# Performance work log

Measured on AMD Instinct MI355X. Metric: run time of the kernel, lower is better.

Reference implementation:

```python
import jax, jax.numpy as jnp
import numpy as np

N_USERS = 50000
N_ENTITIES = 150000
N_NODES = N_USERS + N_ENTITIES
N_EDGES = 3200000
BATCH = 4096
EPS = 1e-12  # F.normalize eps


def setup_inputs() -> dict:
    key = jax.random.key(0)
    ks = jax.random.split(key, 16)
    s = 0.1  # xavier-ish scale for small dims
    return {
        "user_w": jax.random.normal(ks[0], (N_USERS, 64), jnp.float32) * s,
        "entity_w": jax.random.normal(ks[1], (N_ENTITIES, 64), jnp.float32) * s,
        "W1a": jax.random.normal(ks[2], (64, 64), jnp.float32) * s,
        "b1a": jnp.zeros((64,), jnp.float32),
        "W2a": jax.random.normal(ks[3], (64, 64), jnp.float32) * s,
        "b2a": jnp.zeros((64,), jnp.float32),
        "W1b": jax.random.normal(ks[4], (64, 32), jnp.float32) * s,
        "b1b": jnp.zeros((32,), jnp.float32),
        "W2b": jax.random.normal(ks[5], (64, 32), jnp.float32) * s,
        "b2b": jnp.zeros((32,), jnp.float32),
        "values": jax.random.uniform(ks[6], (N_EDGES,), jnp.float32),
        "target": jax.random.randint(ks[7], (N_EDGES,), 0, N_NODES, jnp.int32),
        "neighbor": jax.random.randint(ks[8], (N_EDGES,), 0, N_NODES, jnp.int32),
        "user_ids": jax.random.randint(ks[9], (BATCH,), 0, N_USERS, jnp.int32),
        "pos_item_ids": jax.random.randint(ks[10], (BATCH,), 0, N_ENTITIES, jnp.int32),
        "neg_item_ids": jax.random.randint(ks[11], (BATCH,), 0, N_ENTITIES, jnp.int32),
    }


def _aggregate(features, target, neighbor, values):
    # msg = features[neighbor] * values[:, None]; h_neigh = index_add over target
    msg = features[neighbor] * values[:, None]  # (E, dim)
    return jax.ops.segment_sum(msg, target, num_segments=N_NODES)


def _gnn_layer(features, target, neighbor, values, W1, b1, W2, b2):
    h_neigh = _aggregate(features, target, neighbor, values)
    h = (features + h_neigh) @ W1 + b1 + (features * h_neigh) @ W2 + b2
    return jax.nn.leaky_relu(h, negative_slope=0.01)


def _l2norm(x):
    n = jnp.sqrt(jnp.sum(x * x, axis=1, keepdims=True))
    return x / jnp.maximum(n, EPS)


def reference(user_w, entity_w, W1a, b1a, W2a, b2a, W1b, b1b, W2b, b2b,
              values, target, neighbor, user_ids, pos_item_ids, neg_item_ids):
    all_embed = jnp.concatenate([user_w, entity_w], axis=0)  # (N, 64)
    ego = [all_embed]
    h1 = _l2norm(_gnn_layer(all_embed, target, neighbor, values, W1a, b1a, W2a, b2a))
    ego.append(h1)
    h2 = _l2norm(_gnn_layer(h1, target, neighbor, values, W1b, b1b, W2b, b2b))
    ego.append(h2)
    final_embed = jnp.concatenate(ego, axis=1)  # (N, 160)
    u = final_embed[user_ids]
    pos_i = final_embed[N_USERS + pos_item_ids]
    neg_i = final_embed[N_USERS + neg_item_ids]
    pos_scores = jnp.sum(u * pos_i, axis=1)
    neg_scores = jnp.sum(u * neg_i, axis=1)
    return (pos_scores, neg_scores)
```

## Files before the change

kernel.cpp:

```cpp
#include <hip/hip_runtime.h>

#define N_USERS    50000
#define N_ENTITIES 150000
#define N_NODES_C  200000
#define BATCH_C    4096
#define N_EDGES_C  3200000

#define CHUNK   7168
#define SG_SH   9
#define NSG     391

typedef __attribute__((ext_vector_type(2))) _Float16 h2;
typedef __attribute__((ext_vector_type(8))) _Float16 half8;
typedef __attribute__((ext_vector_type(2))) __fp16 fp16x2_s;
typedef __attribute__((ext_vector_type(4))) float float4v;


__device__ __forceinline__ h2 u2h(unsigned u) {
    union { unsigned u; h2 h; } x; x.u = u; return x.h;
}
__device__ __forceinline__ unsigned pk2h(float a, float b) {
    union { fp16x2_s h; unsigned u; } x;
    x.h = __builtin_amdgcn_cvt_pkrtz(a, b);
    return x.u;
}

__global__ __launch_bounds__(256) void prep_k(const float* __restrict__ uw,
                                              const float* __restrict__ ew,
                                              unsigned short* __restrict__ fb,
                                              const int* __restrict__ target,
                                              int* __restrict__ cntarr,
                                              int* __restrict__ sgtot,
                                              int n_edges, int nchunks)
{
    __shared__ int cnt[NSG];
    int bid = blockIdx.x;
    if (bid < nchunks) {
        int base = bid * CHUNK;
        int ccount = min(CHUNK, n_edges - base);
        for (int i = threadIdx.x; i < NSG; i += 256) cnt[i] = 0;
        __syncthreads();
        for (int i = threadIdx.x; i < ccount; i += 256)
            atomicAdd(&cnt[target[base + i] >> SG_SH], 1);
        __syncthreads();
        for (int i = threadIdx.x; i < NSG; i += 256) {
            cntarr[bid * NSG + i] = cnt[i];
            if (cnt[i]) atomicAdd(&sgtot[i], cnt[i]);
        }
    } else {
        int idx = (bid - nchunks) * 256 + threadIdx.x;
        if (idx >= N_NODES_C * 64) return;
        const int split = N_USERS * 64;
        float x = (idx < split) ? uw[idx] : ew[idx - split];
        _Float16 hx = (_Float16)x;
        fb[idx] = *(unsigned short*)&hx;
    }
}

__global__ __launch_bounds__(512) void scan_k(const int* __restrict__ sgtot,
                                              int* __restrict__ sgoff,
                                              int* __restrict__ sgcur)
{
    __shared__ int part[512];
    int t = threadIdx.x;
    int v = (t < NSG) ? sgtot[t] : 0;
    part[t] = v;
    __syncthreads();
    for (int off = 1; off < 512; off <<= 1) {
        int w = (t >= off) ? part[t - off] : 0;
        __syncthreads();
        part[t] += w;
        __syncthreads();
    }
    if (t < NSG) { sgoff[t] = part[t] - v; sgcur[t] = part[t] - v; }
    if (t == NSG - 1) sgoff[NSG] = part[t];
}

__global__ __launch_bounds__(256) void scatter_k(
    const int* __restrict__ target, const int* __restrict__ neighbor,
    const float* __restrict__ values, const int* __restrict__ cntarr,
    int* __restrict__ sgcur, uint2* __restrict__ tmp2, int n_edges)
{
    __shared__ uint2 buf[CHUNK];
    __shared__ int cnt[NSG], off[NSG], pos[NSG], gbase[NSG];
    int c = blockIdx.x;
    int base = c * CHUNK;
    int ccount = min(CHUNK, n_edges - base);
    for (int i = threadIdx.x; i < NSG; i += 256) {
        int v = cntarr[c * NSG + i];
        cnt[i] = v;
        pos[i] = 0;
        gbase[i] = 0;
    }
    __syncthreads();
    for (int i = threadIdx.x; i < NSG; i += 256)
        if (cnt[i]) gbase[i] = atomicAdd(&sgcur[i], cnt[i]);
    if (threadIdx.x < 64) {
        int l = threadIdx.x;
        const int PER = (NSG + 63) / 64;
        int s0 = l * PER, s1 = min(s0 + PER, NSG);
        int sum = 0;
        for (int i = s0; i < s1; i++) sum += cnt[i];
        int run = sum;
        #pragma unroll
        for (int o = 1; o < 64; o <<= 1) { int v = __shfl_up(run, o); if (l >= o) run += v; }
        int excl = run - sum;
        for (int i = s0; i < s1; i++) { off[i] = excl; excl += cnt[i]; }
    }
    __syncthreads();
    for (int i = threadIdx.x; i < ccount; i += 256) {
        int t  = target[base + i];
        int sg = t >> SG_SH;
        unsigned q = (unsigned)fminf(values[base + i] * 16384.f + 0.5f, 16383.f);
        unsigned w = ((unsigned)neighbor[base + i] << 14) | q;
        int p = off[sg] + atomicAdd(&pos[sg], 1);
        buf[p] = make_uint2(w, (unsigned)t);
    }
    __syncthreads();
    for (int i = threadIdx.x; i < ccount; i += 256) {
        uint2 ed = buf[i];
        int sg = (int)(ed.y >> SG_SH);
        tmp2[(size_t)(gbase[sg] + (i - off[sg]))] = ed;
    }
}

__global__ __launch_bounds__(512) void sort2_k(
    const uint2* __restrict__ tmp2, const int* __restrict__ sgoff,
    int* __restrict__ row_ptr, unsigned* __restrict__ edges)
{
    __shared__ int cnt[512];
    __shared__ int cur[512];
    __shared__ int rp[513];
    int s = blockIdx.x;
    int node0 = s << SG_SH;
    int nn = min(512, N_NODES_C - node0);
    int sgstart = sgoff[s];
    int sgcnt = sgoff[s + 1] - sgstart;
    cnt[threadIdx.x] = 0;
    cur[threadIdx.x] = 0;
    __syncthreads();
    for (int e = threadIdx.x; e < sgcnt; e += 512)
        atomicAdd(&cnt[tmp2[(size_t)sgstart + e].y & 511u], 1);
    __syncthreads();
    if (threadIdx.x < 64) {
        int l = threadIdx.x;
        int s0 = l * 8;
        int vals[8];
        int sum = 0;
        for (int i = 0; i < 8; i++) { vals[i] = cnt[s0 + i]; sum += vals[i]; }
        int run = sum;
        #pragma unroll
        for (int o = 1; o < 64; o <<= 1) { int v = __shfl_up(run, o); if (l >= o) run += v; }
        int excl = run - sum;
        for (int i = 0; i < 8; i++) { rp[s0 + i] = excl; excl += vals[i]; }
        if (l == 63) rp[512] = excl;
    }
    __syncthreads();
    for (int i = threadIdx.x; i < nn; i += 512) row_ptr[node0 + i] = sgstart + rp[i];
    if (s == NSG - 1 && threadIdx.x == 0) row_ptr[N_NODES_C] = sgstart + sgcnt;
    for (int e = threadIdx.x; e < sgcnt; e += 512) {
        uint2 ed = tmp2[(size_t)sgstart + e];
        int tl = (int)(ed.y & 511u);
        int old = atomicAdd(&cur[tl], 1);
        edges[sgstart + rp[tl] + old] = ed.x;
    }
}

#define SPS 136
__global__ __launch_bounds__(512, 6) void layer1_pull_k(
    const unsigned short* __restrict__ fb,
    const int* __restrict__ row_ptr, const unsigned int* __restrict__ edges,
    const float* __restrict__ W1, const float* __restrict__ b1,
    const float* __restrict__ W2, const float* __restrict__ b2,
    _Float16* __restrict__ h1out, int n_nodes)
{
    __shared__ __align__(16) short wt[64 * SPS];
    __shared__ __align__(16) short sp[128 * SPS];
    __shared__ float sbias[64];

    for (int idx = threadIdx.x; idx < 64 * 64; idx += 512) {
        int kp = idx >> 6;
        int n  = idx & 63;
        int k0 = kp * 2, k1 = k0 + 1;
        float w0 = (k0 < 64) ? W1[k0 * 64 + n] : W2[(k0 - 64) * 64 + n];
        float w1 = (k1 < 64) ? W1[k1 * 64 + n] : W2[(k1 - 64) * 64 + n];
        *(unsigned*)&wt[n * SPS + k0] = pk2h(w0, w1);
    }
    if (threadIdx.x < 64) sbias[threadIdx.x] = b1[threadIdx.x] + b2[threadIdx.x];
    __syncthreads();

    int wv   = threadIdx.x >> 6;
    int lane = threadIdx.x & 63;
    int g    = lane >> 4;
    int q    = lane & 15;
    const uint2* fb2 = (const uint2*)fb;

    int nb0 = blockIdx.x * 128;
    const float QS = 1.f / 16384.f;

    for (int i = 0; i < 16; i += 4) {
        int mA = wv * 16 + i;
        int nodeBase = nb0 + mA;

        int es0 = 0, ee0 = 0, es1 = 0, ee1 = 0, es2 = 0, ee2 = 0, es3 = 0, ee3 = 0;
        if (nodeBase     < n_nodes) { es0 = row_ptr[nodeBase];     ee0 = row_ptr[nodeBase + 1]; }
        if (nodeBase + 1 < n_nodes) { es1 = row_ptr[nodeBase + 1]; ee1 = row_ptr[nodeBase + 2]; }
        if (nodeBase + 2 < n_nodes) { es2 = row_ptr[nodeBase + 2]; ee2 = row_ptr[nodeBase + 3]; }
        if (nodeBase + 3 < n_nodes) { es3 = row_ptr[nodeBase + 3]; ee3 = row_ptr[nodeBase + 4]; }

        h2 aLo0 = (h2){0, 0}, aHi0 = (h2){0, 0};
        h2 aLo1 = (h2){0, 0}, aHi1 = (h2){0, 0};
        h2 aLo2 = (h2){0, 0}, aHi2 = (h2){0, 0};
        h2 aLo3 = (h2){0, 0}, aHi3 = (h2){0, 0};

        int b0 = es0, b1c = es1, b2c = es2, b3c = es3;
        while (b0 < ee0 || b1c < ee1 || b2c < ee2 || b3c < ee3) {
            int c0 = ee0 - b0;  c0 = c0 < 0 ? 0 : (c0 > 64 ? 64 : c0);
            int c1 = ee1 - b1c; c1 = c1 < 0 ? 0 : (c1 > 64 ? 64 : c1);
            int c2 = ee2 - b2c; c2 = c2 < 0 ? 0 : (c2 > 64 ? 64 : c2);
            int c3 = ee3 - b3c; c3 = c3 < 0 ? 0 : (c3 > 64 ? 64 : c3);
            unsigned ev0 = (lane < c0) ? edges[b0 + lane]  : 0u;
            unsigned ev1 = (lane < c1) ? edges[b1c + lane] : 0u;
            unsigned ev2 = (lane < c2) ? edges[b2c + lane] : 0u;
            unsigned ev3 = (lane < c3) ? edges[b3c + lane] : 0u;
            int jm0 = (c0 + 3) >> 2;
            int jm1 = (c1 + 3) >> 2;
            int jm2 = (c2 + 3) >> 2;
            int jm3 = (c3 + 3) >> 2;
            int jm = max(max(jm0, jm1), max(jm2, jm3));
            #pragma unroll 4
            for (int j = 0; j < jm; j++) {
                unsigned w0 = (unsigned)__shfl((int)ev0, j * 4 + g);
                unsigned w1 = (unsigned)__shfl((int)ev1, j * 4 + g);
                unsigned w2 = (unsigned)__shfl((int)ev2, j * 4 + g);
                unsigned w3 = (unsigned)__shfl((int)ev3, j * 4 + g);
                uint2 d0 = fb2[(size_t)(w0 >> 14) * 16 + q];
                uint2 d1 = fb2[(size_t)(w1 >> 14) * 16 + q];
                uint2 d2 = fb2[(size_t)(w2 >> 14) * 16 + q];
                uint2 d3 = fb2[(size_t)(w3 >> 14) * 16 + q];
                _Float16 v0 = (_Float16)((float)(w0 & 16383u) * QS);
                _Float16 v1 = (_Float16)((float)(w1 & 16383u) * QS);
                _Float16 v2 = (_Float16)((float)(w2 & 16383u) * QS);
                _Float16 v3 = (_Float16)((float)(w3 & 16383u) * QS);
                h2 vv0 = (h2){v0, v0};
                h2 vv1 = (h2){v1, v1};
                h2 vv2 = (h2){v2, v2};
                h2 vv3 = (h2){v3, v3};
                aLo0 += u2h(d0.x) * vv0;  aHi0 += u2h(d0.y) * vv0;
                aLo1 += u2h(d1.x) * vv1;  aHi1 += u2h(d1.y) * vv1;
                aLo2 += u2h(d2.x) * vv2;  aHi2 += u2h(d2.y) * vv2;
                aLo3 += u2h(d3.x) * vv3;  aHi3 += u2h(d3.y) * vv3;
            }
            b0 += 64; b1c += 64; b2c += 64; b3c += 64;
        }

        float ac[4][4];
        ac[0][0] = (float)aLo0.x; ac[0][1] = (float)aLo0.y; ac[0][2] = (float)aHi0.x; ac[0][3] = (float)aHi0.y;
        ac[1][0] = (float)aLo1.x; ac[1][1] = (float)aLo1.y; ac[1][2] = (float)aHi1.x; ac[1][3] = (float)aHi1.y;
        ac[2][0] = (float)aLo2.x; ac[2][1] = (float)aLo2.y; ac[2][2] = (float)aHi2.x; ac[2][3] = (float)aHi2.y;
        ac[3][0] = (float)aLo3.x; ac[3][1] = (float)aLo3.y; ac[3][2] = (float)aHi3.x; ac[3][3] = (float)aHi3.y;
        #pragma unroll
        for (int s = 0; s < 4; s++)
            #pragma unroll
            for (int c = 0; c < 4; c++) {
                ac[s][c] += __shfl_xor(ac[s][c], 16);
                ac[s][c] += __shfl_xor(ac[s][c], 32);
            }

        int hseg = g >> 1;
        int prod = g & 1;
        int r0 = mA + (hseg << 1);
        int r1 = r0 + 1;
        int nd0 = nb0 + r0, nd1 = nb0 + r1;
        uint2 d0 = make_uint2(0u, 0u), d1 = make_uint2(0u, 0u);
        if (nd0 < n_nodes) d0 = fb2[(size_t)nd0 * 16 + q];
        if (nd1 < n_nodes) d1 = fb2[(size_t)nd1 * 16 + q];
        float a00 = hseg ? ac[2][0] : ac[0][0];
        float a01 = hseg ? ac[2][1] : ac[0][1];
        float a02 = hseg ? ac[2][2] : ac[0][2];
        float a03 = hseg ? ac[2][3] : ac[0][3];
        float a10 = hseg ? ac[3][0] : ac[1][0];
        float a11 = hseg ? ac[3][1] : ac[1][1];
        float a12 = hseg ? ac[3][2] : ac[1][2];
        float a13 = hseg ? ac[3][3] : ac[1][3];
        h2 s0l = u2h(d0.x), s0h = u2h(d0.y);
        h2 s1l = u2h(d1.x), s1h = u2h(d1.y);
        float f00 = (float)s0l.x, f01 = (float)s0l.y, f02 = (float)s0h.x, f03 = (float)s0h.y;
        float f10 = (float)s1l.x, f11 = (float)s1l.y, f12 = (float)s1h.x, f13 = (float)s1h.y;
        float x00 = prod ? f00 * a00 : f00 + a00;
        float x01 = prod ? f01 * a01 : f01 + a01;
        float x02 = prod ? f02 * a02 : f02 + a02;
        float x03 = prod ? f03 * a03 : f03 + a03;
        float x10 = prod ? f10 * a10 : f10 + a10;
        float x11 = prod ? f11 * a11 : f11 + a11;
        float x12 = prod ? f12 * a12 : f12 + a12;
        float x13 = prod ? f13 * a13 : f13 + a13;
        uint2 pk;
        pk.x = pk2h(x00, x01);
        pk.y = pk2h(x02, x03);
        *(uint2*)&sp[r0 * SPS + prod * 64 + q * 4] = pk;
        pk.x = pk2h(x10, x11);
        pk.y = pk2h(x12, x13);
        *(uint2*)&sp[r1 * SPS + prod * 64 + q * 4] = pk;
    }

    __builtin_amdgcn_wave_barrier();
    asm volatile("s_waitcnt lgkmcnt(0)" ::: "memory");
    __builtin_amdgcn_wave_barrier();

    float4v c0, c1, c2, c3;
    {
        float bv0 = sbias[q];
        float bv1 = sbias[16 + q];
        float bv2 = sbias[32 + q];
        float bv3 = sbias[48 + q];
        c0 = (float4v){bv0, bv0, bv0, bv0};
        c1 = (float4v){bv1, bv1, bv1, bv1};
        c2 = (float4v){bv2, bv2, bv2, bv2};
        c3 = (float4v){bv3, bv3, bv3, bv3};
    }
    #pragma unroll
    for (int kk = 0; kk < 4; kk++) {
        int ko = kk * 32 + g * 8;
        half8 a   = *(const half8*)&sp[(wv * 16 + q) * SPS + ko];
        half8 bb0 = *(const half8*)&wt[(q)      * SPS + ko];
        half8 bb1 = *(const half8*)&wt[(16 + q) * SPS + ko];
        half8 bb2 = *(const half8*)&wt[(32 + q) * SPS + ko];
        half8 bb3 = *(const half8*)&wt[(48 + q) * SPS + ko];
        c0 = __builtin_amdgcn_mfma_f32_16x16x32_f16(a, bb0, c0, 0, 0, 0);
        c1 = __builtin_amdgcn_mfma_f32_16x16x32_f16(a, bb1, c1, 0, 0, 0);
        c2 = __builtin_amdgcn_mfma_f32_16x16x32_f16(a, bb2, c2, 0, 0, 0);
        c3 = __builtin_amdgcn_mfma_f32_16x16x32_f16(a, bb3, c3, 0, 0, 0);
    }

    float ss[4];
    #pragma unroll
    for (int r = 0; r < 4; r++) {
        c0[r] = (c0[r] > 0.f) ? c0[r] : 0.01f * c0[r];
        c1[r] = (c1[r] > 0.f) ? c1[r] : 0.01f * c1[r];
        c2[r] = (c2[r] > 0.f) ? c2[r] : 0.01f * c2[r];
        c3[r] = (c3[r] > 0.f) ? c3[r] : 0.01f * c3[r];
        ss[r] = c0[r]*c0[r] + c1[r]*c1[r] + c2[r]*c2[r] + c3[r]*c3[r];
        #pragma unroll
        for (int mm = 1; mm < 16; mm <<= 1) ss[r] += __shfl_xor(ss[r], mm);
        ss[r] = 1.f / fmaxf(sqrtf(ss[r]), 1e-12f);
    }
    #pragma unroll
    for (int r = 0; r < 4; r++) {
        int node_r = nb0 + wv * 16 + g * 4 + r;
        if (node_r >= n_nodes) continue;
        size_t row = (size_t)node_r * 64;
        h1out[row +      q] = (_Float16)(c0[r] * ss[r]);
        h1out[row + 16 + q] = (_Float16)(c1[r] * ss[r]);
        h1out[row + 32 + q] = (_Float16)(c2[r] * ss[r]);
        h1out[row + 48 + q] = (_Float16)(c3[r] * ss[r]);
    }
}

__device__ __forceinline__ float layer2_row(
    const _Float16* __restrict__ h1,
    const int* __restrict__ row_ptr, const unsigned int* __restrict__ edges,
    const float* sW1, const float* sW2, const float* sb,
    int node, int lane)
{
    int es = row_ptr[node];
    int ee = row_ptr[node + 1];
    const float QS = 1.f / 16384.f;
    float g = 0.f;
    for (int base = es; base < ee; base += 64) {
        int cnt = min(64, ee - base);
        unsigned ev = (lane < cnt) ? edges[base + lane] : 0u;
        int j = 0;
        for (; j + 4 <= cnt; j += 4) {
            unsigned e0 = (unsigned)__shfl((int)ev, j);
            unsigned e1 = (unsigned)__shfl((int)ev, j + 1);
            unsigned e2 = (unsigned)__shfl((int)ev, j + 2);
            unsigned e3 = (unsigned)__shfl((int)ev, j + 3);
            float f0 = (float)h1[(size_t)(e0 >> 14) * 64 + lane];
            float f1 = (float)h1[(size_t)(e1 >> 14) * 64 + lane];
            float f2 = (float)h1[(size_t)(e2 >> 14) * 64 + lane];
            float f3 = (float)h1[(size_t)(e3 >> 14) * 64 + lane];
            g += (float)(e0 & 16383u) * QS * f0 + (float)(e1 & 16383u) * QS * f1
               + (float)(e2 & 16383u) * QS * f2 + (float)(e3 & 16383u) * QS * f3;
        }
        for (; j < cnt; j++) {
            unsigned e0 = (unsigned)__shfl((int)ev, j);
            float f0 = (float)h1[(size_t)(e0 >> 14) * 64 + lane];
            g += (float)(e0 & 16383u) * QS * f0;
        }
    }
    float f = (float)h1[(size_t)node * 64 + lane];
    float s = f + g;
    float p = f * g;
    int j = lane & 31;
    float acc = sb[j];
    #pragma unroll
    for (int k = 0; k < 64; k++) {
        float sk = __shfl(s, k);
        float pk = __shfl(p, k);
        acc += sk * sW1[k * 32 + j] + pk * sW2[k * 32 + j];
    }
    acc = (acc > 0.f) ? acc : 0.01f * acc;
    float sq = acc * acc;
    #pragma unroll
    for (int m = 1; m < 32; m <<= 1) sq += __shfl_xor(sq, m);
    return acc / fmaxf(sqrtf(sq), 1e-12f);
}

__global__ __launch_bounds__(256) void score_k(
    const float* __restrict__ uw, const float* __restrict__ ew,
    const _Float16* __restrict__ h1,
    const int* __restrict__ row_ptr, const unsigned int* __restrict__ edges,
    const float* __restrict__ W1b, const float* __restrict__ b1b,
    const float* __restrict__ W2b, const float* __restrict__ b2b,
    const int* __restrict__ uid, const int* __restrict__ pid,
    const int* __restrict__ nid, float* __restrict__ out)
{
    __shared__ float sW1[64 * 32];
    __shared__ float sW2[64 * 32];
    __shared__ float sb[32];
    for (int i = threadIdx.x; i < 64 * 32; i += 256) { sW1[i] = W1b[i]; sW2[i] = W2b[i]; }
    if (threadIdx.x < 32) sb[threadIdx.x] = b1b[threadIdx.x] + b2b[threadIdx.x];
    __syncthreads();

    int wave = threadIdx.x >> 6;
    int lane = threadIdx.x & 63;
    int i = blockIdx.x * 4 + wave;
    if (i >= BATCH_C) return;

    int un = uid[i];
    int pe = pid[i];
    int ne = nid[i];
    int pn = N_USERS + pe;
    int nn = N_USERS + ne;

    float acc01p, acc01n;
    {
        float u  = uw[(size_t)un * 64 + lane];
        float pv = ew[(size_t)pe * 64 + lane];
        float nv = ew[(size_t)ne * 64 + lane];
        acc01p = u * pv;
        acc01n = u * nv;
        float u1 = (float)h1[(size_t)un * 64 + lane];
        acc01p += u1 * (float)h1[(size_t)pn * 64 + lane];
        acc01n += u1 * (float)h1[(size_t)nn * 64 + lane];
    }

    float h2u = layer2_row(h1, row_ptr, edges, sW1, sW2, sb, un, lane);
    float h2p = layer2_row(h1, row_ptr, edges, sW1, sW2, sb, pn, lane);
    float h2n = layer2_row(h1, row_ptr, edges, sW1, sW2, sb, nn, lane);
    float p2 = h2u * h2p;
    float n2 = h2u * h2n;
    #pragma unroll
    for (int m = 1; m < 32; m <<= 1) { p2 += __shfl_xor(p2, m); n2 += __shfl_xor(n2, m); }

    #pragma unroll
    for (int m = 1; m < 64; m <<= 1) { acc01p += __shfl_xor(acc01p, m); acc01n += __shfl_xor(acc01n, m); }

    if (lane == 0) {
        out[i]           = acc01p + p2;
        out[BATCH_C + i] = acc01n + n2;
    }
}

extern "C" void kernel_launch(void* const* d_in, const int* in_sizes, int n_in,
                              void* d_out, int out_size, void* d_ws, size_t ws_size,
                              hipStream_t stream) {
    const float* uw   = (const float*)d_in[0];
    const float* ew   = (const float*)d_in[1];
    const float* W1a  = (const float*)d_in[2];
    const float* b1a  = (const float*)d_in[3];
    const float* W2a  = (const float*)d_in[4];
    const float* b2a  = (const float*)d_in[5];
    const float* W1b  = (const float*)d_in[6];
    const float* b1b  = (const float*)d_in[7];
    const float* W2b  = (const float*)d_in[8];
    const float* b2b  = (const float*)d_in[9];
    const float* values   = (const float*)d_in[10];
    const int*   target   = (const int*)d_in[11];
    const int*   neighbor = (const int*)d_in[12];
    const int*   uid  = (const int*)d_in[13];
    const int*   pid  = (const int*)d_in[14];
    const int*   nid  = (const int*)d_in[15];

    const int n_edges = in_sizes[10];

    char* ws = (char*)d_ws;
    int*  row_ptr    = (int*)ws;   ws += 801792;
    int*  cntarr     = (int*)ws;   ws += 704512;
    int*  sgtot      = (int*)ws;   ws += 4096;
    int*  sgoff      = (int*)ws;   ws += 4096;
    int*  sgcur      = (int*)ws;   ws += 4096;
    unsigned int*   edges = (unsigned int*)ws;   ws += (size_t)N_EDGES_C * 4;
    unsigned short* fb    = (unsigned short*)ws; ws += (size_t)N_NODES_C * 64 * 2;
    uint2*          tmp2  = (uint2*)ws;
    _Float16*       h1    = (_Float16*)ws;

    const int layer_blocks = (N_NODES_C + 127) / 128;
    const int conv_blocks  = (N_NODES_C * 64 + 255) / 256;
    const int nchunks      = (n_edges + CHUNK - 1) / CHUNK;

    hipMemsetAsync(sgtot, 0, (NSG + 1) * sizeof(int), stream);

    prep_k<<<nchunks + conv_blocks, 256, 0, stream>>>(uw, ew, fb, target,
                                                      cntarr, sgtot, n_edges, nchunks);

    scan_k<<<1, 512, 0, stream>>>(sgtot, sgoff, sgcur);
    scatter_k<<<nchunks, 256, 0, stream>>>(target, neighbor, values, cntarr, sgcur, tmp2, n_edges);
    sort2_k<<<NSG, 512, 0, stream>>>(tmp2, sgoff, row_ptr, edges);

    layer1_pull_k<<<layer_blocks, 512, 0, stream>>>(fb, row_ptr, edges,
                                                    W1a, b1a, W2a, b2a, h1, N_NODES_C);

    score_k<<<BATCH_C / 4, 256, 0, stream>>>(uw, ew, h1, row_ptr, edges,
                                             W1b, b1b, W2b, b2b,
                                             uid, pid, nid, (float*)d_out);
}
```

Measured before the change: 346.8 us.

## Vectorize fp16 conversion, cache sorted edges in LDS, store edge values as fp16 bits

The fp32 to fp16 embedding conversion now handles 8 elements per thread with vector loads and packed converts, which cuts the conversion block count. The second sort pass stages each segment's edges in shared memory during the counting pass, so tmp2 is not read from global memory a second time. Edge weights are stored as the low 14 bits of their fp16 encoding rather than a fixed-point quantization, so the layer kernels can rebuild the half value with bit operations instead of a convert and multiply. This relies on values lying in [0,1), whose fp16 encodings fit in 14 bits, and the larger shared-memory use in sort2_k may lower its occupancy.

```diff
diff --git a/kernel.cpp b/kernel.cpp
--- a/kernel.cpp
+++ b/kernel.cpp
@@ -9,6 +9,7 @@
 #define CHUNK   7168
 #define SG_SH   9
 #define NSG     391
+#define S2CAP   12288
 
 typedef __attribute__((ext_vector_type(2))) _Float16 h2;
 typedef __attribute__((ext_vector_type(8))) _Float16 half8;
@@ -24,7 +25,13 @@
     x.h = __builtin_amdgcn_cvt_pkrtz(a, b);
     return x.u;
 }
-
+__device__ __forceinline__ float val_f32(unsigned e) {
+    union { unsigned short s; _Float16 h; } x;
+    x.s = (unsigned short)(e & 0x3FFFu);
+    return (float)x.h;
+}
+
+#define CONVB 6250
 __global__ __launch_bounds__(256) void prep_k(const float* __restrict__ uw,
                                               const float* __restrict__ ew,
                                               unsigned short* __restrict__ fb,
@@ -48,12 +55,17 @@
             if (cnt[i]) atomicAdd(&sgtot[i], cnt[i]);
         }
     } else {
-        int idx = (bid - nchunks) * 256 + threadIdx.x;
-        if (idx >= N_NODES_C * 64) return;
+        int base8 = ((bid - nchunks) * 256 + threadIdx.x) * 8;
         const int split = N_USERS * 64;
-        float x = (idx < split) ? uw[idx] : ew[idx - split];
-        _Float16 hx = (_Float16)x;
-        fb[idx] = *(unsigned short*)&hx;
+        const float* src = (base8 < split) ? (uw + base8) : (ew + (base8 - split));
+        float4 a = *(const float4*)src;
+        float4 b = *(const float4*)(src + 4);
+        uint4 o;
+        o.x = pk2h(a.x, a.y);
+        o.y = pk2h(a.z, a.w);
+        o.z = pk2h(b.x, b.y);
+        o.w = pk2h(b.z, b.w);
+        *(uint4*)(fb + base8) = o;
     }
 }
 
@@ -111,8 +123,10 @@
     for (int i = threadIdx.x; i < ccount; i += 256) {
         int t  = target[base + i];
         int sg = t >> SG_SH;
-        unsigned q = (unsigned)fminf(values[base + i] * 16384.f + 0.5f, 16383.f);
-        unsigned w = ((unsigned)neighbor[base + i] << 14) | q;
+        _Float16 hv = (_Float16)values[base + i];
+        unsigned short hb;
+        __builtin_memcpy(&hb, &hv, 2);
+        unsigned w = ((unsigned)neighbor[base + i] << 14) | (unsigned)(hb & 0x3FFFu);
         int p = off[sg] + atomicAdd(&pos[sg], 1);
         buf[p] = make_uint2(w, (unsigned)t);
     }
@@ -128,6 +142,8 @@
     const uint2* __restrict__ tmp2, const int* __restrict__ sgoff,
     int* __restrict__ row_ptr, unsigned* __restrict__ edges)
 {
+    __shared__ unsigned ebuf[S2CAP];
+    __shared__ unsigned short tbuf[S2CAP];
     __shared__ int cnt[512];
     __shared__ int cur[512];
     __shared__ int rp[513];
@@ -139,8 +155,12 @@
     cnt[threadIdx.x] = 0;
     cur[threadIdx.x] = 0;
     __syncthreads();
-    for (int e = threadIdx.x; e < sgcnt; e += 512)
-        atomicAdd(&cnt[tmp2[(size_t)sgstart + e].y & 511u], 1);
+    for (int e = threadIdx.x; e < sgcnt; e += 512) {
+        uint2 ed = tmp2[(size_t)sgstart + e];
+        int tl = (int)(ed.y & 511u);
+        atomicAdd(&cnt[tl], 1);
+        if (e < S2CAP) { ebuf[e] = ed.x; tbuf[e] = (unsigned short)tl; }
+    }
     __syncthreads();
     if (threadIdx.x < 64) {
         int l = threadIdx.x;
@@ -158,7 +178,13 @@
     __syncthreads();
     for (int i = threadIdx.x; i < nn; i += 512) row_ptr[node0 + i] = sgstart + rp[i];
     if (s == NSG - 1 && threadIdx.x == 0) row_ptr[N_NODES_C] = sgstart + sgcnt;
-    for (int e = threadIdx.x; e < sgcnt; e += 512) {
+    int lim = min(sgcnt, S2CAP);
+    for (int e = threadIdx.x; e < lim; e += 512) {
+        int tl = tbuf[e];
+        int old = atomicAdd(&cur[tl], 1);
+        edges[sgstart + rp[tl] + old] = ebuf[e];
+    }
+    for (int e = S2CAP + threadIdx.x; e < sgcnt; e += 512) {
         uint2 ed = tmp2[(size_t)sgstart + e];
         int tl = (int)(ed.y & 511u);
         int old = atomicAdd(&cur[tl], 1);
@@ -196,7 +222,6 @@
     const uint2* fb2 = (const uint2*)fb;
 
     int nb0 = blockIdx.x * 128;
-    const float QS = 1.f / 16384.f;
 
     for (int i = 0; i < 16; i += 4) {
         int mA = wv * 16 + i;
@@ -238,14 +263,14 @@
                 uint2 d1 = fb2[(size_t)(w1 >> 14) * 16 + q];
                 uint2 d2 = fb2[(size_t)(w2 >> 14) * 16 + q];
                 uint2 d3 = fb2[(size_t)(w3 >> 14) * 16 + q];
-                _Float16 v0 = (_Float16)((float)(w0 & 16383u) * QS);
-                _Float16 v1 = (_Float16)((float)(w1 & 16383u) * QS);
-                _Float16 v2 = (_Float16)((float)(w2 & 16383u) * QS);
-                _Float16 v3 = (_Float16)((float)(w3 & 16383u) * QS);
-                h2 vv0 = (h2){v0, v0};
-                h2 vv1 = (h2){v1, v1};
-                h2 vv2 = (h2){v2, v2};
-                h2 vv3 = (h2){v3, v3};
+                unsigned vb0 = w0 & 0x3FFFu;
+                unsigned vb1 = w1 & 0x3FFFu;
+                unsigned vb2 = w2 & 0x3FFFu;
+                unsigned vb3 = w3 & 0x3FFFu;
+                h2 vv0 = u2h(vb0 | (vb0 << 16));
+                h2 vv1 = u2h(vb1 | (vb1 << 16));
+                h2 vv2 = u2h(vb2 | (vb2 << 16));
+                h2 vv3 = u2h(vb3 | (vb3 << 16));
                 aLo0 += u2h(d0.x) * vv0;  aHi0 += u2h(d0.y) * vv0;
                 aLo1 += u2h(d1.x) * vv1;  aHi1 += u2h(d1.y) * vv1;
                 aLo2 += u2h(d2.x) * vv2;  aHi2 += u2h(d2.y) * vv2;
@@ -365,7 +390,6 @@
 {
     int es = row_ptr[node];
     int ee = row_ptr[node + 1];
-    const float QS = 1.f / 16384.f;
     float g = 0.f;
     for (int base = es; base < ee; base += 64) {
         int cnt = min(64, ee - base);
@@ -380,13 +404,13 @@
             float f1 = (float)h1[(size_t)(e1 >> 14) * 64 + lane];
             float f2 = (float)h1[(size_t)(e2 >> 14) * 64 + lane];
             float f3 = (float)h1[(size_t)(e3 >> 14) * 64 + lane];
-            g += (float)(e0 & 16383u) * QS * f0 + (float)(e1 & 16383u) * QS * f1
-               + (float)(e2 & 16383u) * QS * f2 + (float)(e3 & 16383u) * QS * f3;
+            g += val_f32(e0) * f0 + val_f32(e1) * f1
+               + val_f32(e2) * f2 + val_f32(e3) * f3;
         }
         for (; j < cnt; j++) {
             unsigned e0 = (unsigned)__shfl((int)ev, j);
             float f0 = (float)h1[(size_t)(e0 >> 14) * 64 + lane];
-            g += (float)(e0 & 16383u) * QS * f0;
+            g += val_f32(e0) * f0;
         }
     }
     float f = (float)h1[(size_t)node * 64 + lane];
@@ -497,13 +521,12 @@
     _Float16*       h1    = (_Float16*)ws;
 
     const int layer_blocks = (N_NODES_C + 127) / 128;
-    const int conv_blocks  = (N_NODES_C * 64 + 255) / 256;
     const int nchunks      = (n_edges + CHUNK - 1) / CHUNK;
 
     hipMemsetAsync(sgtot, 0, (NSG + 1) * sizeof(int), stream);
 
-    prep_k<<<nchunks + conv_blocks, 256, 0, stream>>>(uw, ew, fb, target,
-                                                      cntarr, sgtot, n_edges, nchunks);
+    prep_k<<<nchunks + CONVB, 256, 0, stream>>>(uw, ew, fb, target,
+                                                cntarr, sgtot, n_edges, nchunks);
 
     scan_k<<<1, 512, 0, stream>>>(sgtot, sgoff, sgcur);
     scatter_k<<<nchunks, 256, 0, stream>>>(target, neighbor, values, cntarr, sgcur, tmp2, n_edges);
```

Measured after the change: 335.2 us. -3.4%, faster.
